# Kernel tuning notes

Hardware: AMD Instinct MI355X
Metric: run time of the kernel (lower is better)

## Reference

```python
import jax, jax.numpy as jnp
import numpy as np

N, F, H, O = 16384, 64, 128, 512

def setup_inputs() -> dict:
    key = jax.random.key(0)
    ks = jax.random.split(key, 5)
    # PyTorch Linear default init: U(-1/sqrt(fan_in), 1/sqrt(fan_in))
    lim1 = 1.0  # fan_in = 1 for Linear(1, H)
    lim2 = 1.0 / np.sqrt(H)
    x = jax.random.normal(ks[0], (N, F), dtype=jnp.float32)
    W1 = jax.random.uniform(ks[1], (F, H), minval=-lim1, maxval=lim1, dtype=jnp.float32)
    b1 = jax.random.uniform(ks[2], (F, H), minval=-lim1, maxval=lim1, dtype=jnp.float32)
    W2 = jax.random.uniform(ks[3], (F, H, O), minval=-lim2, maxval=lim2, dtype=jnp.float32)
    b2 = jax.random.uniform(ks[4], (F, O), minval=-lim2, maxval=lim2, dtype=jnp.float32)
    return {"x": x, "W1": W1, "b1": b1, "W2": W2, "b2": b2}

def reference(x, W1, b1, W2, b2):
    # Per-feature MLP: h_f = W2_f @ elu(x_f * w1_f + b1_f) + b2_f, summed over f.
    # pre: [N, F, H] = outer-product of each scalar feature with its W1 row
    pre = x[:, :, None] * W1[None, :, :] + b1[None, :, :]
    a = jax.nn.elu(pre)                                  # [N, F, H]
    h = jnp.einsum('nfh,fho->no', a, W2)                 # sum over f and h
    h = h + jnp.sum(b2, axis=0)[None, :]                 # biases summed over F
    return h / jnp.sqrt(jnp.float32(F))
```

## Files before the change

### kernel.cpp

```cpp
#include <hip/hip_runtime.h>
#include <cstdint>

#define NROWS 16384
#define FDIM 64
#define HDIM 128
#define ODIM 512
#define KDIM 8192

#define BM 64
#define BN 256
#define BK 64

typedef short bf16x8 __attribute__((ext_vector_type(8)));
typedef float f32x4 __attribute__((ext_vector_type(4)));
typedef uint32_t u32x4 __attribute__((ext_vector_type(4)));

__device__ __forceinline__ uint16_t rne_bf16(float f) {
  uint32_t u = __builtin_bit_cast(uint32_t, f);
  u += 0x7fffu + ((u >> 16) & 1u);
  return (uint16_t)(u >> 16);
}

__global__ void prep_w2t(const float* __restrict__ W2, uint16_t* __restrict__ W2T) {
  __shared__ float tile[64][65];
  const int k0 = blockIdx.x * 64;
  const int o0 = blockIdx.y * 64;
  const int tx = threadIdx.x;
  const int ty = threadIdx.y;
#pragma unroll
  for (int j = 0; j < 8; ++j)
    tile[ty + 8 * j][tx] = W2[(size_t)(k0 + ty + 8 * j) * ODIM + o0 + tx];
  __syncthreads();
#pragma unroll
  for (int j = 0; j < 8; ++j)
    W2T[(size_t)(o0 + ty + 8 * j) * KDIM + k0 + tx] = rne_bf16(tile[tx][ty + 8 * j]);
}

__global__ void prep_small(const float* __restrict__ W1, const float* __restrict__ b1,
                           const float* __restrict__ b2, uint16_t* __restrict__ w1bf,
                           uint16_t* __restrict__ b1bf, float* __restrict__ b2sum) {
  const int t = blockIdx.x * 256 + threadIdx.x;
  w1bf[t] = rne_bf16(W1[t]);
  b1bf[t] = rne_bf16(b1[t]);
  if (t < ODIM) {
    float s = 0.f;
#pragma unroll
    for (int f = 0; f < FDIM; ++f) s += b2[(size_t)f * ODIM + t];
    b2sum[t] = s;
  }
}

__global__ __launch_bounds__(256, 3) void mlp_gemm(
    const float* __restrict__ x, const uint16_t* __restrict__ w1bf,
    const uint16_t* __restrict__ b1bf, const uint16_t* __restrict__ W2T,
    const float* __restrict__ b2sum, float* __restrict__ out) {
  __shared__ __align__(16) uint16_t As[BM * BK];
  __shared__ __align__(16) uint16_t Bs[BN * BK];

  const int tid = threadIdx.x;
  const int bid = blockIdx.x;
  const int o0 = (bid & 1) * BN;
  const int m0 = (bid >> 1) * BM;

  const int wid = tid >> 6;
  const int lane = tid & 63;
  const int wn = wid * 64;
  const int q = lane >> 4;
  const int r = lane & 15;

  const int ar = tid >> 3;
  const int ac = tid & 7;
  const int brow = lane >> 3;
  const int bcg = (lane & 7) ^ brow;

  f32x4 acc[4][4];
#pragma unroll
  for (int i = 0; i < 4; ++i)
#pragma unroll
    for (int j = 0; j < 4; ++j) acc[i][j] = {0.f, 0.f, 0.f, 0.f};

  for (int f = 0; f < FDIM; ++f) {
    float xv[2];
#pragma unroll
    for (int i = 0; i < 2; ++i)
      xv[i] = x[(size_t)(m0 + i * 32 + ar) * FDIM + f];

#pragma unroll
    for (int half = 0; half < 2; ++half) {
      const int kk = f * 2 + half;
      __syncthreads();

#pragma unroll
      for (int j = 0; j < 8; ++j) {
        const int chunk = wid * 8 + j;
        const uint16_t* gp =
            W2T + (size_t)(o0 + chunk * 8 + brow) * KDIM + kk * BK + bcg * 8;
        uint16_t* lp = &Bs[chunk * 512];
        __builtin_amdgcn_global_load_lds(
            (const __attribute__((address_space(1))) uint32_t*)gp,
            (__attribute__((address_space(3))) uint32_t*)lp, 16, 0, 0);
      }

      const int hoff = half * 64 + ac * 8;
      u32x4 w1d = *(const u32x4*)(w1bf + f * HDIM + hoff);
      u32x4 b1d = *(const u32x4*)(b1bf + f * HDIM + hoff);
      float w1f[8], b1f[8];
#pragma unroll
      for (int p = 0; p < 4; ++p) {
        w1f[2 * p]     = __builtin_bit_cast(float, w1d[p] << 16);
        w1f[2 * p + 1] = __builtin_bit_cast(float, w1d[p] & 0xffff0000u);
        b1f[2 * p]     = __builtin_bit_cast(float, b1d[p] << 16);
        b1f[2 * p + 1] = __builtin_bit_cast(float, b1d[p] & 0xffff0000u);
      }
#pragma unroll
      for (int i = 0; i < 2; ++i) {
        const int m = i * 32 + ar;
        u32x4 ov;
#pragma unroll
        for (int p = 0; p < 4; ++p) {
          float plo = fmaf(xv[i], w1f[2 * p], b1f[2 * p]);
          float phi = fmaf(xv[i], w1f[2 * p + 1], b1f[2 * p + 1]);
          float elo = plo > 0.f ? plo : __expf(plo) - 1.f;
          float ehi = phi > 0.f ? phi : __expf(phi) - 1.f;
          ov[p] = __builtin_amdgcn_perm(__builtin_bit_cast(uint32_t, ehi),
                                        __builtin_bit_cast(uint32_t, elo),
                                        0x07060302u);
        }
        *(u32x4*)&As[m * BK + ((ac ^ (m & 7)) * 8)] = ov;
      }
      __syncthreads();

#pragma unroll
      for (int kc = 0; kc < 2; ++kc) {
        bf16x8 af[4], bfr[4];
        const int cg = kc * 4 + q;
#pragma unroll
        for (int mt = 0; mt < 4; ++mt) {
          const int row = mt * 16 + r;
          af[mt] = *(const bf16x8*)&As[row * BK + ((cg ^ (row & 7)) * 8)];
        }
#pragma unroll
        for (int nt = 0; nt < 4; ++nt) {
          const int row = wn + nt * 16 + r;
          bfr[nt] = *(const bf16x8*)&Bs[row * BK + ((cg ^ (row & 7)) * 8)];
        }
#pragma unroll
        for (int mt = 0; mt < 4; ++mt)
#pragma unroll
          for (int nt = 0; nt < 4; ++nt)
            acc[mt][nt] = __builtin_amdgcn_mfma_f32_16x16x32_bf16(
                af[mt], bfr[nt], acc[mt][nt], 0, 0, 0);
      }
    }
  }

  float bsv[4];
#pragma unroll
  for (int nt = 0; nt < 4; ++nt) bsv[nt] = b2sum[o0 + wn + nt * 16 + r];
#pragma unroll
  for (int mt = 0; mt < 4; ++mt)
#pragma unroll
    for (int nt = 0; nt < 4; ++nt)
#pragma unroll
      for (int v = 0; v < 4; ++v) {
        const int row = m0 + mt * 16 + q * 4 + v;
        const int col = o0 + wn + nt * 16 + r;
        out[(size_t)row * ODIM + col] = (acc[mt][nt][v] + bsv[nt]) * 0.125f;
      }
}

extern "C" void kernel_launch(void* const* d_in, const int* in_sizes, int n_in,
                              void* d_out, int out_size, void* d_ws, size_t ws_size,
                              hipStream_t stream) {
  const float* x  = (const float*)d_in[0];
  const float* W1 = (const float*)d_in[1];
  const float* b1 = (const float*)d_in[2];
  const float* W2 = (const float*)d_in[3];
  const float* b2 = (const float*)d_in[4];
  float* out = (float*)d_out;

  char* ws = (char*)d_ws;
  float*    b2sum = (float*)ws;
  uint16_t* w1bf  = (uint16_t*)(ws + 4096);
  uint16_t* b1bf  = (uint16_t*)(ws + 4096 + 16384);
  uint16_t* W2T   = (uint16_t*)(ws + 65536);

  prep_w2t<<<dim3(KDIM / 64, ODIM / 64), dim3(64, 8), 0, stream>>>(W2, W2T);
  prep_small<<<32, 256, 0, stream>>>(W1, b1, b2, w1bf, b1bf, b2sum);
  mlp_gemm<<<(NROWS / BM) * (ODIM / BN), 256, 0, stream>>>(x, w1bf, b1bf, W2T,
                                                           b2sum, out);
}
```

Before: 256.0 us.

## Double-buffer LDS tiles, enlarge block to 128x256 with 8 waves, grouped tile order

Restructures the fused ELU+GEMM kernel to use double-buffered A/B LDS tiles so the next K-step's W2 loads and ELU generation overlap with MFMA compute on the current step, halving syncs per step. The block tile grows to 128x256 with 512 threads in a 2x4 wave grid, and blocks are remapped into groups of four M-tiles per N-half to improve W2 reuse in L2. W1/b1 are now read directly in fp32 instead of via a bf16 prep kernel, and ELU becomes branchless. LDS use doubles and larger tiles reduce block count to 256, which may lower occupancy.

```diff
diff --git a/kernel.cpp b/kernel.cpp
--- a/kernel.cpp
+++ b/kernel.cpp
@@ -7,9 +7,10 @@
 #define ODIM 512
 #define KDIM 8192
 
-#define BM 64
+#define BM 128
 #define BN 256
 #define BK 64
+#define NSTEPS (KDIM / BK)
 
 typedef short bf16x8 __attribute__((ext_vector_type(8)));
 typedef float f32x4 __attribute__((ext_vector_type(4)));
@@ -36,35 +37,33 @@
     W2T[(size_t)(o0 + ty + 8 * j) * KDIM + k0 + tx] = rne_bf16(tile[tx][ty + 8 * j]);
 }
 
-__global__ void prep_small(const float* __restrict__ W1, const float* __restrict__ b1,
-                           const float* __restrict__ b2, uint16_t* __restrict__ w1bf,
-                           uint16_t* __restrict__ b1bf, float* __restrict__ b2sum) {
+__global__ void prep_b2sum(const float* __restrict__ b2, float* __restrict__ b2sum) {
   const int t = blockIdx.x * 256 + threadIdx.x;
-  w1bf[t] = rne_bf16(W1[t]);
-  b1bf[t] = rne_bf16(b1[t]);
-  if (t < ODIM) {
-    float s = 0.f;
+  float s = 0.f;
 #pragma unroll
-    for (int f = 0; f < FDIM; ++f) s += b2[(size_t)f * ODIM + t];
-    b2sum[t] = s;
-  }
+  for (int f = 0; f < FDIM; ++f) s += b2[(size_t)f * ODIM + t];
+  b2sum[t] = s;
 }
 
-__global__ __launch_bounds__(256, 3) void mlp_gemm(
-    const float* __restrict__ x, const uint16_t* __restrict__ w1bf,
-    const uint16_t* __restrict__ b1bf, const uint16_t* __restrict__ W2T,
+__global__ __launch_bounds__(512, 2) void mlp_gemm(
+    const float* __restrict__ x, const float* __restrict__ W1,
+    const float* __restrict__ b1, const uint16_t* __restrict__ W2T,
     const float* __restrict__ b2sum, float* __restrict__ out) {
-  __shared__ __align__(16) uint16_t As[BM * BK];
-  __shared__ __align__(16) uint16_t Bs[BN * BK];
+  __shared__ __align__(16) uint16_t As0[BM * BK];
+  __shared__ __align__(16) uint16_t As1[BM * BK];
+  __shared__ __align__(16) uint16_t Bs0[BN * BK];
+  __shared__ __align__(16) uint16_t Bs1[BN * BK];
 
   const int tid = threadIdx.x;
   const int bid = blockIdx.x;
-  const int o0 = (bid & 1) * BN;
-  const int m0 = (bid >> 1) * BM;
+  const int g = bid & 7;
+  const int o0 = (g >> 2) * BN;
+  const int m0 = ((bid >> 3) * 4 + (g & 3)) * BM;
 
   const int wid = tid >> 6;
   const int lane = tid & 63;
-  const int wn = wid * 64;
+  const int wm = wid >> 2;
+  const int wni = wid & 3;
   const int q = lane >> 4;
   const int r = lane & 15;
 
@@ -73,98 +72,109 @@
   const int brow = lane >> 3;
   const int bcg = (lane & 7) ^ brow;
 
+  const float* xp0 = x + (size_t)(m0 + ar) * FDIM;
+  const float* xp1 = x + (size_t)(m0 + 64 + ar) * FDIM;
+  const int aw0 = ar * BK + ((ac ^ (ar & 7)) * 8);
+  const int aw1 = (ar + 64) * BK + ((ac ^ (ar & 7)) * 8);
+
   f32x4 acc[4][4];
 #pragma unroll
   for (int i = 0; i < 4; ++i)
 #pragma unroll
     for (int j = 0; j < 4; ++j) acc[i][j] = {0.f, 0.f, 0.f, 0.f};
 
-  for (int f = 0; f < FDIM; ++f) {
-    float xv[2];
+  auto stage = [&](uint16_t* Ab, uint16_t* Bb, int kk) {
 #pragma unroll
-    for (int i = 0; i < 2; ++i)
-      xv[i] = x[(size_t)(m0 + i * 32 + ar) * FDIM + f];
+    for (int j = 0; j < 4; ++j) {
+      const int chunk = wid * 4 + j;
+      const uint16_t* gp =
+          W2T + (size_t)(o0 + chunk * 8 + brow) * KDIM + kk * BK + bcg * 8;
+      uint16_t* lp = Bb + chunk * 512;
+      __builtin_amdgcn_global_load_lds(
+          (const __attribute__((address_space(1))) uint32_t*)gp,
+          (__attribute__((address_space(3))) uint32_t*)lp, 16, 0, 0);
+    }
+    const int f = kk >> 1;
+    const int hoff = (kk & 1) * 64 + ac * 8;
+    const float xv0 = xp0[f];
+    const float xv1 = xp1[f];
+    float w1f[8], b1f[8];
+    *(f32x4*)&w1f[0] = *(const f32x4*)(W1 + (size_t)f * HDIM + hoff);
+    *(f32x4*)&w1f[4] = *(const f32x4*)(W1 + (size_t)f * HDIM + hoff + 4);
+    *(f32x4*)&b1f[0] = *(const f32x4*)(b1 + (size_t)f * HDIM + hoff);
+    *(f32x4*)&b1f[4] = *(const f32x4*)(b1 + (size_t)f * HDIM + hoff + 4);
+    u32x4 ov0, ov1;
+#pragma unroll
+    for (int p = 0; p < 4; ++p) {
+      float a0 = fmaf(xv0, w1f[2 * p], b1f[2 * p]);
+      float a1 = fmaf(xv0, w1f[2 * p + 1], b1f[2 * p + 1]);
+      float c0 = fmaf(xv1, w1f[2 * p], b1f[2 * p]);
+      float c1 = fmaf(xv1, w1f[2 * p + 1], b1f[2 * p + 1]);
+      float e0 = fmaxf(a0, __expf(fminf(a0, 0.f)) - 1.f);
+      float e1 = fmaxf(a1, __expf(fminf(a1, 0.f)) - 1.f);
+      float g0 = fmaxf(c0, __expf(fminf(c0, 0.f)) - 1.f);
+      float g1 = fmaxf(c1, __expf(fminf(c1, 0.f)) - 1.f);
+      ov0[p] = __builtin_amdgcn_perm(__builtin_bit_cast(uint32_t, e1),
+                                     __builtin_bit_cast(uint32_t, e0), 0x07060302u);
+      ov1[p] = __builtin_amdgcn_perm(__builtin_bit_cast(uint32_t, g1),
+                                     __builtin_bit_cast(uint32_t, g0), 0x07060302u);
+    }
+    *(u32x4*)(Ab + aw0) = ov0;
+    *(u32x4*)(Ab + aw1) = ov1;
+  };
 
+  auto compute = [&](const uint16_t* Ab, const uint16_t* Bb) {
 #pragma unroll
-    for (int half = 0; half < 2; ++half) {
-      const int kk = f * 2 + half;
-      __syncthreads();
-
+    for (int kc = 0; kc < 2; ++kc) {
+      const int cg = kc * 4 + q;
+      bf16x8 af[4], bfr[4];
 #pragma unroll
-      for (int j = 0; j < 8; ++j) {
-        const int chunk = wid * 8 + j;
-        const uint16_t* gp =
-            W2T + (size_t)(o0 + chunk * 8 + brow) * KDIM + kk * BK + bcg * 8;
-        uint16_t* lp = &Bs[chunk * 512];
-        __builtin_amdgcn_global_load_lds(
-            (const __attribute__((address_space(1))) uint32_t*)gp,
-            (__attribute__((address_space(3))) uint32_t*)lp, 16, 0, 0);
-      }
-
-      const int hoff = half * 64 + ac * 8;
-      u32x4 w1d = *(const u32x4*)(w1bf + f * HDIM + hoff);
-      u32x4 b1d = *(const u32x4*)(b1bf + f * HDIM + hoff);
-      float w1f[8], b1f[8];
-#pragma unroll
-      for (int p = 0; p < 4; ++p) {
-        w1f[2 * p]     = __builtin_bit_cast(float, w1d[p] << 16);
-        w1f[2 * p + 1] = __builtin_bit_cast(float, w1d[p] & 0xffff0000u);
-        b1f[2 * p]     = __builtin_bit_cast(float, b1d[p] << 16);
-        b1f[2 * p + 1] = __builtin_bit_cast(float, b1d[p] & 0xffff0000u);
+      for (int mt = 0; mt < 4; ++mt) {
+        const int row = wm * 64 + mt * 16 + r;
+        af[mt] = *(const bf16x8*)&Ab[row * BK + ((cg ^ (row & 7)) * 8)];
       }
 #pragma unroll
-      for (int i = 0; i < 2; ++i) {
-        const int m = i * 32 + ar;
-        u32x4 ov;
+      for (int nt = 0; nt < 4; ++nt) {
+        const int row = wni * 64 + nt * 16 + r;
+        bfr[nt] = *(const bf16x8*)&Bb[row * BK + ((cg ^ (row & 7)) * 8)];
+      }
 #pragma unroll
-        for (int p = 0; p < 4; ++p) {
-          float plo = fmaf(xv[i], w1f[2 * p], b1f[2 * p]);
-          float phi = fmaf(xv[i], w1f[2 * p + 1], b1f[2 * p + 1]);
-          float elo = plo > 0.f ? plo : __expf(plo) - 1.f;
-          float ehi = phi > 0.f ? phi : __expf(phi) - 1.f;
-          ov[p] = __builtin_amdgcn_perm(__builtin_bit_cast(uint32_t, ehi),
-                                        __builtin_bit_cast(uint32_t, elo),
-                                        0x07060302u);
-        }
-        *(u32x4*)&As[m * BK + ((ac ^ (m & 7)) * 8)] = ov;
-      }
-      __syncthreads();
+      for (int mt = 0; mt < 4; ++mt)
+#pragma unroll
+        for (int nt = 0; nt < 4; ++nt)
+          acc[mt][nt] = __builtin_amdgcn_mfma_f32_16x16x32_bf16(
+              af[mt], bfr[nt], acc[mt][nt], 0, 0, 0);
+    }
+  };
 
-#pragma unroll
-      for (int kc = 0; kc < 2; ++kc) {
-        bf16x8 af[4], bfr[4];
-        const int cg = kc * 4 + q;
-#pragma unroll
-        for (int mt = 0; mt < 4; ++mt) {
-          const int row = mt * 16 + r;
-          af[mt] = *(const bf16x8*)&As[row * BK + ((cg ^ (row & 7)) * 8)];
-        }
-#pragma unroll
-        for (int nt = 0; nt < 4; ++nt) {
-          const int row = wn + nt * 16 + r;
-          bfr[nt] = *(const bf16x8*)&Bs[row * BK + ((cg ^ (row & 7)) * 8)];
-        }
-#pragma unroll
-        for (int mt = 0; mt < 4; ++mt)
-#pragma unroll
-          for (int nt = 0; nt < 4; ++nt)
-            acc[mt][nt] = __builtin_amdgcn_mfma_f32_16x16x32_bf16(
-                af[mt], bfr[nt], acc[mt][nt], 0, 0, 0);
-      }
-    }
+  stage(As0, Bs0, 0);
+  __syncthreads();
+
+#pragma unroll 1
+  for (int kk = 0; kk < NSTEPS - 2; kk += 2) {
+    stage(As1, Bs1, kk + 1);
+    compute(As0, Bs0);
+    __syncthreads();
+    stage(As0, Bs0, kk + 2);
+    compute(As1, Bs1);
+    __syncthreads();
   }
+  stage(As1, Bs1, NSTEPS - 1);
+  compute(As0, Bs0);
+  __syncthreads();
+  compute(As1, Bs1);
 
   float bsv[4];
 #pragma unroll
-  for (int nt = 0; nt < 4; ++nt) bsv[nt] = b2sum[o0 + wn + nt * 16 + r];
+  for (int nt = 0; nt < 4; ++nt) bsv[nt] = b2sum[o0 + wni * 64 + nt * 16 + r];
 #pragma unroll
   for (int mt = 0; mt < 4; ++mt)
 #pragma unroll
     for (int nt = 0; nt < 4; ++nt)
 #pragma unroll
       for (int v = 0; v < 4; ++v) {
-        const int row = m0 + mt * 16 + q * 4 + v;
-        const int col = o0 + wn + nt * 16 + r;
+        const int row = m0 + wm * 64 + mt * 16 + q * 4 + v;
+        const int col = o0 + wni * 64 + nt * 16 + r;
         out[(size_t)row * ODIM + col] = (acc[mt][nt][v] + bsv[nt]) * 0.125f;
       }
 }
@@ -181,12 +191,9 @@
 
   char* ws = (char*)d_ws;
   float*    b2sum = (float*)ws;
-  uint16_t* w1bf  = (uint16_t*)(ws + 4096);
-  uint16_t* b1bf  = (uint16_t*)(ws + 4096 + 16384);
   uint16_t* W2T   = (uint16_t*)(ws + 65536);
 
   prep_w2t<<<dim3(KDIM / 64, ODIM / 64), dim3(64, 8), 0, stream>>>(W2, W2T);
-  prep_small<<<32, 256, 0, stream>>>(W1, b1, b2, w1bf, b1bf, b2sum);
-  mlp_gemm<<<(NROWS / BM) * (ODIM / BN), 256, 0, stream>>>(x, w1bf, b1bf, W2T,
-                                                           b2sum, out);
+  prep_b2sum<<<2, 256, 0, stream>>>(b2, b2sum);
+  mlp_gemm<<<256, 512, 0, stream>>>(x, W1, b1, W2T, b2sum, out);
 }
```

Result: slower. 271.1 us (+5.9%).

## Double-buffer LDS tiles and prefetch operands to overlap loads with MFMA

Applied to the files above, without the earlier changes.

Splits the A and B shared-memory tiles into two buffers and restructures the K loop into a software pipeline. The next stage's W2T global-to-LDS copy, the ELU computation of A and the register prefetch of x/W1/b1 are issued while MFMAs run on the current buffer. This cuts the loop to one barrier per stage, removing the pair of barriers and the exposed load latency of the old loop. It doubles the LDS footprint and lowers the launch-bounds occupancy hint from 3 to 2 blocks per CU.

```diff
diff --git a/kernel.cpp b/kernel.cpp
--- a/kernel.cpp
+++ b/kernel.cpp
@@ -10,6 +10,7 @@
 #define BM 64
 #define BN 256
 #define BK 64
+#define NST 128
 
 typedef short bf16x8 __attribute__((ext_vector_type(8)));
 typedef float f32x4 __attribute__((ext_vector_type(4)));
@@ -50,12 +51,19 @@
   }
 }
 
-__global__ __launch_bounds__(256, 3) void mlp_gemm(
+struct Pref {
+  u32x4 w1d, b1d;
+  float xv0, xv1;
+};
+
+__global__ __launch_bounds__(256, 2) void mlp_gemm(
     const float* __restrict__ x, const uint16_t* __restrict__ w1bf,
     const uint16_t* __restrict__ b1bf, const uint16_t* __restrict__ W2T,
     const float* __restrict__ b2sum, float* __restrict__ out) {
-  __shared__ __align__(16) uint16_t As[BM * BK];
-  __shared__ __align__(16) uint16_t Bs[BN * BK];
+  __shared__ __align__(16) uint16_t As0[BM * BK];
+  __shared__ __align__(16) uint16_t As1[BM * BK];
+  __shared__ __align__(16) uint16_t Bs0[BN * BK];
+  __shared__ __align__(16) uint16_t Bs1[BN * BK];
 
   const int tid = threadIdx.x;
   const int bid = blockIdx.x;
@@ -79,80 +87,109 @@
 #pragma unroll
     for (int j = 0; j < 4; ++j) acc[i][j] = {0.f, 0.f, 0.f, 0.f};
 
-  for (int f = 0; f < FDIM; ++f) {
-    float xv[2];
-#pragma unroll
-    for (int i = 0; i < 2; ++i)
-      xv[i] = x[(size_t)(m0 + i * 32 + ar) * FDIM + f];
-
-#pragma unroll
-    for (int half = 0; half < 2; ++half) {
-      const int kk = f * 2 + half;
-      __syncthreads();
-
-#pragma unroll
-      for (int j = 0; j < 8; ++j) {
-        const int chunk = wid * 8 + j;
-        const uint16_t* gp =
-            W2T + (size_t)(o0 + chunk * 8 + brow) * KDIM + kk * BK + bcg * 8;
-        uint16_t* lp = &Bs[chunk * 512];
-        __builtin_amdgcn_global_load_lds(
-            (const __attribute__((address_space(1))) uint32_t*)gp,
-            (__attribute__((address_space(3))) uint32_t*)lp, 16, 0, 0);
-      }
-
-      const int hoff = half * 64 + ac * 8;
-      u32x4 w1d = *(const u32x4*)(w1bf + f * HDIM + hoff);
-      u32x4 b1d = *(const u32x4*)(b1bf + f * HDIM + hoff);
-      float w1f[8], b1f[8];
+  auto ldops = [&](Pref& P, int s) {
+    const int f = s >> 1;
+    const int hoff = (s & 1) * 64 + ac * 8;
+    P.w1d = *(const u32x4*)(w1bf + f * HDIM + hoff);
+    P.b1d = *(const u32x4*)(b1bf + f * HDIM + hoff);
+    P.xv0 = x[(size_t)(m0 + ar) * FDIM + f];
+    P.xv1 = x[(size_t)(m0 + 32 + ar) * FDIM + f];
+  };
+
+  auto stageB = [&](uint16_t* Bb, int kk) {
+#pragma unroll
+    for (int j = 0; j < 8; ++j) {
+      const int chunk = wid * 8 + j;
+      const uint16_t* gp =
+          W2T + (size_t)(o0 + chunk * 8 + brow) * KDIM + kk * BK + bcg * 8;
+      uint16_t* lp = Bb + chunk * 512;
+      __builtin_amdgcn_global_load_lds(
+          (const __attribute__((address_space(1))) uint32_t*)gp,
+          (__attribute__((address_space(3))) uint32_t*)lp, 16, 0, 0);
+    }
+  };
+
+  auto eluA = [&](uint16_t* Ab, const Pref& P) {
+    float w1f[8], b1f[8];
+#pragma unroll
+    for (int p = 0; p < 4; ++p) {
+      w1f[2 * p]     = __builtin_bit_cast(float, P.w1d[p] << 16);
+      w1f[2 * p + 1] = __builtin_bit_cast(float, P.w1d[p] & 0xffff0000u);
+      b1f[2 * p]     = __builtin_bit_cast(float, P.b1d[p] << 16);
+      b1f[2 * p + 1] = __builtin_bit_cast(float, P.b1d[p] & 0xffff0000u);
+    }
+#pragma unroll
+    for (int i = 0; i < 2; ++i) {
+      const float xv = i ? P.xv1 : P.xv0;
+      const int m = i * 32 + ar;
+      u32x4 ov;
 #pragma unroll
       for (int p = 0; p < 4; ++p) {
-        w1f[2 * p]     = __builtin_bit_cast(float, w1d[p] << 16);
-        w1f[2 * p + 1] = __builtin_bit_cast(float, w1d[p] & 0xffff0000u);
-        b1f[2 * p]     = __builtin_bit_cast(float, b1d[p] << 16);
-        b1f[2 * p + 1] = __builtin_bit_cast(float, b1d[p] & 0xffff0000u);
-      }
-#pragma unroll
-      for (int i = 0; i < 2; ++i) {
-        const int m = i * 32 + ar;
-        u32x4 ov;
-#pragma unroll
-        for (int p = 0; p < 4; ++p) {
-          float plo = fmaf(xv[i], w1f[2 * p], b1f[2 * p]);
-          float phi = fmaf(xv[i], w1f[2 * p + 1], b1f[2 * p + 1]);
-          float elo = plo > 0.f ? plo : __expf(plo) - 1.f;
-          float ehi = phi > 0.f ? phi : __expf(phi) - 1.f;
-          ov[p] = __builtin_amdgcn_perm(__builtin_bit_cast(uint32_t, ehi),
-                                        __builtin_bit_cast(uint32_t, elo),
-                                        0x07060302u);
-        }
-        *(u32x4*)&As[m * BK + ((ac ^ (m & 7)) * 8)] = ov;
-      }
-      __syncthreads();
-
-#pragma unroll
-      for (int kc = 0; kc < 2; ++kc) {
-        bf16x8 af[4], bfr[4];
-        const int cg = kc * 4 + q;
-#pragma unroll
-        for (int mt = 0; mt < 4; ++mt) {
-          const int row = mt * 16 + r;
-          af[mt] = *(const bf16x8*)&As[row * BK + ((cg ^ (row & 7)) * 8)];
-        }
-#pragma unroll
-        for (int nt = 0; nt < 4; ++nt) {
-          const int row = wn + nt * 16 + r;
-          bfr[nt] = *(const bf16x8*)&Bs[row * BK + ((cg ^ (row & 7)) * 8)];
-        }
-#pragma unroll
-        for (int mt = 0; mt < 4; ++mt)
-#pragma unroll
-          for (int nt = 0; nt < 4; ++nt)
-            acc[mt][nt] = __builtin_amdgcn_mfma_f32_16x16x32_bf16(
-                af[mt], bfr[nt], acc[mt][nt], 0, 0, 0);
-      }
-    }
+        float plo = fmaf(xv, w1f[2 * p], b1f[2 * p]);
+        float phi = fmaf(xv, w1f[2 * p + 1], b1f[2 * p + 1]);
+        float elo = plo > 0.f ? plo : __expf(plo) - 1.f;
+        float ehi = phi > 0.f ? phi : __expf(phi) - 1.f;
+        ov[p] = __builtin_amdgcn_perm(__builtin_bit_cast(uint32_t, ehi),
+                                      __builtin_bit_cast(uint32_t, elo),
+                                      0x07060302u);
+      }
+      *(u32x4*)&Ab[m * BK + ((ac ^ (m & 7)) * 8)] = ov;
+    }
+  };
+
+  auto compute = [&](const uint16_t* Ab, const uint16_t* Bb) {
+#pragma unroll
+    for (int kc = 0; kc < 2; ++kc) {
+      bf16x8 af[4], bfr[4];
+      const int cg = kc * 4 + q;
+#pragma unroll
+      for (int mt = 0; mt < 4; ++mt) {
+        const int row = mt * 16 + r;
+        af[mt] = *(const bf16x8*)&Ab[row * BK + ((cg ^ (row & 7)) * 8)];
+      }
+#pragma unroll
+      for (int nt = 0; nt < 4; ++nt) {
+        const int row = wn + nt * 16 + r;
+        bfr[nt] = *(const bf16x8*)&Bb[row * BK + ((cg ^ (row & 7)) * 8)];
+      }
+#pragma unroll
+      for (int mt = 0; mt < 4; ++mt)
+#pragma unroll
+        for (int nt = 0; nt < 4; ++nt)
+          acc[mt][nt] = __builtin_amdgcn_mfma_f32_16x16x32_bf16(
+              af[mt], bfr[nt], acc[mt][nt], 0, 0, 0);
+    }
+  };
+
+  Pref P0, P1;
+
+  ldops(P0, 0);
+  __builtin_amdgcn_sched_barrier(0);
+  stageB(Bs0, 0);
+  eluA(As0, P0);
+  ldops(P1, 1);
+  __syncthreads();
+
+#pragma unroll 1
+  for (int kk = 0; kk < NST - 2; kk += 2) {
+    ldops(P0, kk + 2);
+    __builtin_amdgcn_sched_barrier(0);
+    stageB(Bs1, kk + 1);
+    eluA(As1, P1);
+    compute(As0, Bs0);
+    __syncthreads();
+    ldops(P1, kk + 3);
+    __builtin_amdgcn_sched_barrier(0);
+    stageB(Bs0, kk + 2);
+    eluA(As0, P0);
+    compute(As1, Bs1);
+    __syncthreads();
   }
+  stageB(Bs1, NST - 1);
+  eluA(As1, P1);
+  compute(As0, Bs0);
+  __syncthreads();
+  compute(As1, Bs1);
 
   float bsv[4];
 #pragma unroll
```

Measured after the change: 252.8 us. No clear change (-1.3%).
